# Performance work log

Measured on AMD Instinct MI355X. Metric: run time of the kernel, lower is better.

## Reference

```python
import jax, jax.numpy as jnp
import numpy as np

N, E = 100000, 640000
H, EDGE_D, ATOM_D, RD, L = 128, 10, 25, 64, 4


def _gelu(t):
    return jax.nn.gelu(t, approximate=True)  # tanh approximation, matches torch GELU(approximate='tanh')


def _mlp2(t, w1, b1, w2, b2):
    return _gelu(t @ w1 + b1) @ w2 + b2


def setup_inputs() -> dict:
    key = jax.random.key(0)
    ks = iter(jax.random.split(key, 64))
    s = 0.05
    d = {}
    d['x'] = jax.random.normal(next(ks), (N, ATOM_D), jnp.float32)
    d['edge_index'] = jax.random.randint(next(ks), (2, E), 0, N, jnp.int32)
    d['edge_attr'] = jax.random.normal(next(ks), (E, EDGE_D), jnp.float32)
    d['enc_w1'] = jax.random.normal(next(ks), (ATOM_D, H)) * s
    d['enc_b1'] = jnp.zeros((H,))
    d['enc_w2'] = jax.random.normal(next(ks), (H, H)) * s
    d['enc_b2'] = jnp.zeros((H,))
    d['edge_w1'] = jax.random.normal(next(ks), (L, EDGE_D, H)) * s
    d['edge_b1'] = jnp.zeros((L, H))
    d['edge_w2'] = jax.random.normal(next(ks), (L, H, H)) * s
    d['edge_b2'] = jnp.zeros((L, H))
    d['msg_w1'] = jax.random.normal(next(ks), (L, H, H)) * s
    d['msg_b1'] = jnp.zeros((L, H))
    d['msg_w2'] = jax.random.normal(next(ks), (L, H, H)) * s
    d['msg_b2'] = jnp.zeros((L, H))
    d['gate_w'] = jax.random.normal(next(ks), (L, 2 * H, H)) * s
    d['gate_b'] = jnp.zeros((L, H))
    d['ln_g'] = jnp.ones((L, H))
    d['ln_b'] = jnp.zeros((L, H))
    for name in ('ion', 'pka', 'acid'):
        d[name + '_w1'] = jax.random.normal(next(ks), (H, RD)) * s
        d[name + '_b1'] = jnp.zeros((RD,))
        d[name + '_w2'] = jax.random.normal(next(ks), (RD, 1)) * s
        d[name + '_b2'] = jnp.zeros((1,))
    return d


def reference(x, edge_index, edge_attr, enc_w1, enc_b1, enc_w2, enc_b2,
              edge_w1, edge_b1, edge_w2, edge_b2,
              msg_w1, msg_b1, msg_w2, msg_b2,
              gate_w, gate_b, ln_g, ln_b,
              ion_w1, ion_b1, ion_w2, ion_b2,
              pka_w1, pka_b1, pka_w2, pka_b2,
              acid_w1, acid_b1, acid_w2, acid_b2):
    src, dst = edge_index[0], edge_index[1]
    n = x.shape[0]
    h = _mlp2(x, enc_w1, enc_b1, enc_w2, enc_b2)  # [N, H]
    ones_e = jnp.ones((src.shape[0],), x.dtype)
    count = jnp.clip(jax.ops.segment_sum(ones_e, dst, num_segments=n), 1.0)[:, None]  # [N,1]
    for i in range(L):
        ew = _mlp2(edge_attr, edge_w1[i], edge_b1[i], edge_w2[i], edge_b2[i])  # [E, H]
        msg = _mlp2(h[src], msg_w1[i], msg_b1[i], msg_w2[i], msg_b2[i]) * ew   # [E, H]
        agg = jax.ops.segment_sum(msg, dst, num_segments=n) / count           # [N, H] mean agg
        gate = jax.nn.sigmoid(jnp.concatenate([h, agg], axis=-1) @ gate_w[i] + gate_b[i])
        h = h + gate * agg
        mu = jnp.mean(h, axis=-1, keepdims=True)
        var = jnp.mean(jnp.square(h - mu), axis=-1, keepdims=True)
        h = (h - mu) * jax.lax.rsqrt(var + 1e-5) * ln_g[i] + ln_b[i]
    ion = _mlp2(h, ion_w1, ion_b1, ion_w2, ion_b2)
    pka = _mlp2(h, pka_w1, pka_b1, pka_w2, pka_b2)
    acid = _mlp2(h, acid_w1, acid_b1, acid_w2, acid_b2)
    return (ion, pka, acid)
```

## Files before the change

### kernel.cpp

```cpp
#include <hip/hip_runtime.h>
#include <math.h>

#define NN 100000
#define NN2 100032
#define NE 640000
#define H 128
#define AD 25
#define ED 10
#define RD 64
#define NL 4
#define NB_E (NE / 64 + 1)
#define NSB ((NN + 255) / 256)
#define CAP 256

typedef short bfrag __attribute__((ext_vector_type(8)));
typedef float floatx4 __attribute__((ext_vector_type(4)));
typedef unsigned short ushort;

#define MFMA(a, b, c) __builtin_amdgcn_mfma_f32_16x16x32_bf16(a, b, c, 0, 0, 0)

__device__ __forceinline__ ushort f2bf(float f) {
    unsigned u = __float_as_uint(f);
    unsigned r = (u + 0x7FFFu + ((u >> 16) & 1u)) >> 16;
    return (ushort)r;
}
__device__ __forceinline__ float bf2f(ushort b) {
    return __uint_as_float(((unsigned)b) << 16);
}
__device__ __forceinline__ float gelu_t(float x) {
    float u = 0.7978845608028654f * (x + 0.044715f * x * x * x);
    float e = __expf(2.0f * u);
    float th = 1.0f - 2.0f / (e + 1.0f);
    return 0.5f * x * (1.0f + th);
}
__device__ __forceinline__ float sigm(float x) {
    return 1.0f / (1.0f + __expf(-x));
}

__global__ void k_wtall(ushort* __restrict__ wt,
                        const float* __restrict__ s0, const float* __restrict__ s1,
                        const float* __restrict__ s2, const float* __restrict__ s3,
                        const float* __restrict__ s4, const float* __restrict__ s5,
                        const float* __restrict__ s6, const float* __restrict__ s7,
                        const float* __restrict__ s8, const float* __restrict__ s9) {
    int idx = blockIdx.x * 256 + threadIdx.x;
    const float* src;
    int Ks, N, Kd, off;
    if (idx < 4096)        { src = s0; Ks = 25;  N = 128; Kd = 32;  off = 0; }
    else if (idx < 20480)  { src = s1; Ks = 128; N = 128; Kd = 128; off = 4096; }
    else if (idx < 36864)  { src = s2; Ks = 10;  N = 128; Kd = 32;  off = 20480; }
    else if (idx < 102400) { src = s3; Ks = 128; N = 128; Kd = 128; off = 36864; }
    else if (idx < 167936) { src = s4; Ks = 128; N = 128; Kd = 128; off = 102400; }
    else if (idx < 233472) { src = s5; Ks = 128; N = 128; Kd = 128; off = 167936; }
    else if (idx < 364544) { src = s6; Ks = 256; N = 128; Kd = 256; off = 233472; }
    else if (idx < 372736) { src = s7; Ks = 128; N = 64;  Kd = 128; off = 364544; }
    else if (idx < 380928) { src = s8; Ks = 128; N = 64;  Kd = 128; off = 372736; }
    else if (idx < 389120) { src = s9; Ks = 128; N = 64;  Kd = 128; off = 380928; }
    else return;
    int lidx = idx - off;
    int nk = N * Kd;
    int b = lidx / nk;
    int rem = lidx - b * nk;
    int n = rem / Kd, k = rem - n * Kd;
    float v = (k < Ks) ? src[((size_t)b * Ks + k) * N + n] : 0.0f;
    wt[idx] = f2bf(v);
}

__global__ void k_cvt(const float* __restrict__ src, ushort* __restrict__ dst,
                      int rs, int Ks, int Kd, int total) {
    for (int idx = blockIdx.x * 256 + threadIdx.x; idx < total; idx += gridDim.x * 256) {
        int r = idx / Kd, k = idx - r * Kd;
        dst[idx] = (r < rs && k < Ks) ? f2bf(src[(size_t)r * Ks + k]) : 0;
    }
}
__global__ void k_cvtperm(const float* __restrict__ ea, const int* __restrict__ perm,
                          ushort* __restrict__ out) {
    int j = blockIdx.x * 256 + threadIdx.x;
    if (j >= NE) return;
    const float* src = ea + (size_t)perm[j] * ED;
    unsigned u[8];
#pragma unroll
    for (int k = 0; k < 5; ++k)
        u[k] = (unsigned)f2bf(src[2 * k]) | ((unsigned)f2bf(src[2 * k + 1]) << 16);
    u[5] = u[6] = u[7] = 0u;
    uint4* o = (uint4*)(out + (size_t)j * 16);
    uint4 a; a.x = u[0]; a.y = u[1]; a.z = u[2]; a.w = u[3];
    uint4 b; b.x = u[4]; b.y = u[5]; b.z = u[6]; b.w = u[7];
    o[0] = a; o[1] = b;
}

__global__ void k_init3(int* __restrict__ hist, int* __restrict__ nf,
                        int* __restrict__ nl) {
    int i = blockIdx.x * 256 + threadIdx.x;
    if (i < NN) hist[i] = 0;
    if (i < NB_E) { nf[i] = 0x7fffffff; nl[i] = -1; }
}
__global__ void k_hist(const int* __restrict__ ei, int* __restrict__ hist) {
    int e = blockIdx.x * 256 + threadIdx.x;
    if (e < NE) atomicAdd(&hist[ei[NE + e]], 1);
}
__global__ void k_scan1(const int* __restrict__ hist, int* __restrict__ incl,
                        int* __restrict__ bsum) {
    __shared__ int s[256];
    int tid = threadIdx.x;
    int i = blockIdx.x * 256 + tid;
    s[tid] = (i < NN) ? hist[i] : 0;
    __syncthreads();
    for (int off = 1; off < 256; off <<= 1) {
        int t = (tid >= off) ? s[tid - off] : 0;
        __syncthreads();
        s[tid] += t;
        __syncthreads();
    }
    if (i < NN) incl[i] = s[tid];
    if (tid == 255) bsum[blockIdx.x] = s[255];
}
__global__ void k_scan2(int* __restrict__ bsum) {
    __shared__ int s[512];
    int tid = threadIdx.x;
    s[tid] = (tid < NSB) ? bsum[tid] : 0;
    __syncthreads();
    for (int off = 1; off < 512; off <<= 1) {
        int t = (tid >= off) ? s[tid - off] : 0;
        __syncthreads();
        s[tid] += t;
        __syncthreads();
    }
    if (tid < NSB) bsum[tid] = (tid > 0) ? s[tid - 1] : 0;
}
__global__ void k_scan3(const int* __restrict__ hist, const int* __restrict__ incl,
                        const int* __restrict__ bsum, int* __restrict__ row_ptr) {
    int i = blockIdx.x * 256 + threadIdx.x;
    if (i < NN) row_ptr[i] = bsum[blockIdx.x] + incl[i] - hist[i];
    if (i == 0) row_ptr[NN] = NE;
}
__global__ void k_scatter(const int* __restrict__ ei, int* __restrict__ cursor,
                          int* __restrict__ perm) {
    int e = blockIdx.x * 256 + threadIdx.x;
    if (e < NE) {
        int d = ei[NE + e];
        int pos = atomicAdd(&cursor[d], 1);
        perm[pos] = e;
    }
}
__global__ void k_blockrange(const int* __restrict__ row_ptr, int* __restrict__ nf,
                             int* __restrict__ nl) {
    int n = blockIdx.x * 256 + threadIdx.x;
    if (n < NN) {
        int b = row_ptr[n] >> 6;
        atomicMin(&nf[b], n);
        atomicMax(&nl[b], n);
    }
}

__global__ void __launch_bounds__(256)
k_encmsg(const ushort* __restrict__ xbf, ushort* __restrict__ hbf,
         ushort* __restrict__ mbf,
         const ushort* __restrict__ EW1t, const float* __restrict__ EB1,
         const ushort* __restrict__ EW2t, const float* __restrict__ EB2,
         const ushort* __restrict__ MW1t, const float* __restrict__ MB1,
         const ushort* __restrict__ MW2t, const float* __restrict__ MB2) {
    __shared__ ushort sH[64 * 136];
    const int tid = threadIdx.x;
    const int w = tid >> 6, lane = tid & 63, lr = lane & 15, lg = lane >> 4;
    const int rowB = blockIdx.x * 64 + w * 16 + lr;
    ushort* sHrow = sH + (w * 16 + lr) * 136;

    bfrag bv0 = *(const bfrag*)(xbf + (size_t)rowB * 32 + lg * 8);
    floatx4 acc[8];
#pragma unroll
    for (int t = 0; t < 8; ++t) acc[t] = (floatx4){0.f, 0.f, 0.f, 0.f};
#pragma unroll
    for (int t = 0; t < 8; ++t) {
        bfrag av = *(const bfrag*)(EW1t + (t * 16 + lr) * 32 + lg * 8);
        acc[t] = MFMA(av, bv0, acc[t]);
    }
#pragma unroll
    for (int t = 0; t < 8; ++t) {
        const float4 b1 = *(const float4*)(EB1 + t * 16 + lg * 4);
        float h0 = gelu_t(acc[t][0] + b1.x), h1 = gelu_t(acc[t][1] + b1.y);
        float h2 = gelu_t(acc[t][2] + b1.z), h3 = gelu_t(acc[t][3] + b1.w);
        uint2 p;
        p.x = (unsigned)f2bf(h0) | ((unsigned)f2bf(h1) << 16);
        p.y = (unsigned)f2bf(h2) | ((unsigned)f2bf(h3) << 16);
        *(uint2*)(sHrow + t * 16 + lg * 4) = p;
    }
#pragma unroll
    for (int t = 0; t < 8; ++t) acc[t] = (floatx4){0.f, 0.f, 0.f, 0.f};
#pragma unroll
    for (int kb = 0; kb < 4; ++kb) {
        bfrag av = *(const bfrag*)(sHrow + kb * 32 + lg * 8);
#pragma unroll
        for (int t = 0; t < 8; ++t) {
            bfrag bw = *(const bfrag*)(EW2t + (t * 16 + lr) * 128 + kb * 32 + lg * 8);
            acc[t] = MFMA(bw, av, acc[t]);
        }
    }
#pragma unroll
    for (int t = 0; t < 8; ++t) {
        const float4 b2 = *(const float4*)(EB2 + t * 16 + lg * 4);
        uint2 p;
        p.x = (unsigned)f2bf(acc[t][0] + b2.x) |
              ((unsigned)f2bf(acc[t][1] + b2.y) << 16);
        p.y = (unsigned)f2bf(acc[t][2] + b2.z) |
              ((unsigned)f2bf(acc[t][3] + b2.w) << 16);
        if (rowB < NN) *(uint2*)(hbf + (size_t)rowB * 128 + t * 16 + lg * 4) = p;
        *(uint2*)(sHrow + t * 16 + lg * 4) = p;
    }
#pragma unroll
    for (int t = 0; t < 8; ++t) acc[t] = (floatx4){0.f, 0.f, 0.f, 0.f};
#pragma unroll
    for (int kb = 0; kb < 4; ++kb) {
        bfrag bv = *(const bfrag*)(sHrow + kb * 32 + lg * 8);
#pragma unroll
        for (int t = 0; t < 8; ++t) {
            bfrag av = *(const bfrag*)(MW1t + (t * 16 + lr) * 128 + kb * 32 + lg * 8);
            acc[t] = MFMA(av, bv, acc[t]);
        }
    }
#pragma unroll
    for (int t = 0; t < 8; ++t) {
        const float4 b1 = *(const float4*)(MB1 + t * 16 + lg * 4);
        float h0 = gelu_t(acc[t][0] + b1.x), h1 = gelu_t(acc[t][1] + b1.y);
        float h2 = gelu_t(acc[t][2] + b1.z), h3 = gelu_t(acc[t][3] + b1.w);
        uint2 p;
        p.x = (unsigned)f2bf(h0) | ((unsigned)f2bf(h1) << 16);
        p.y = (unsigned)f2bf(h2) | ((unsigned)f2bf(h3) << 16);
        *(uint2*)(sHrow + t * 16 + lg * 4) = p;
    }
#pragma unroll
    for (int t = 0; t < 8; ++t) acc[t] = (floatx4){0.f, 0.f, 0.f, 0.f};
#pragma unroll
    for (int kb = 0; kb < 4; ++kb) {
        bfrag av = *(const bfrag*)(sHrow + kb * 32 + lg * 8);
#pragma unroll
        for (int t = 0; t < 8; ++t) {
            bfrag bw = *(const bfrag*)(MW2t + (t * 16 + lr) * 128 + kb * 32 + lg * 8);
            acc[t] = MFMA(bw, av, acc[t]);
        }
    }
    if (rowB < NN) {
        ushort* orow = mbf + (size_t)rowB * 128;
#pragma unroll
        for (int t = 0; t < 8; ++t) {
            const float4 b2 = *(const float4*)(MB2 + t * 16 + lg * 4);
            uint2 p;
            p.x = (unsigned)f2bf(acc[t][0] + b2.x) |
                  ((unsigned)f2bf(acc[t][1] + b2.y) << 16);
            p.y = (unsigned)f2bf(acc[t][2] + b2.z) |
                  ((unsigned)f2bf(acc[t][3] + b2.w) << 16);
            *(uint2*)(orow + t * 16 + lg * 4) = p;
        }
    }
}

__global__ void __launch_bounds__(256)
k_ew(const ushort* __restrict__ eap, ushort* __restrict__ ewp, int S,
     const ushort* __restrict__ W1t, const float* __restrict__ B1,
     const ushort* __restrict__ W2t, const float* __restrict__ B2) {
    __shared__ ushort sea[128 * 40];
    __shared__ ushort sH[4][16 * 136];
    const int tid = threadIdx.x;
    const int w = tid >> 6, lane = tid & 63, lr = lane & 15, lg = lane >> 4;
    const int jl0 = blockIdx.x * 128;

    {
        int r = tid >> 1, half = tid & 1;
        int j = S + jl0 + r;
        uint4 z; z.x = z.y = z.z = z.w = 0u;
        uint4 v = z;
        if (j < NE) v = *(const uint4*)(eap + (size_t)j * 16 + half * 8);
        *(uint4*)(sea + r * 40 + half * 8) = v;
        *(uint4*)(sea + r * 40 + 16 + half * 8) = z;
    }
    bfrag av1[8];
#pragma unroll
    for (int t = 0; t < 8; ++t)
        av1[t] = *(const bfrag*)(W1t + (t * 16 + lr) * 32 + lg * 8);
    __syncthreads();

    for (int rt = 0; rt < 2; ++rt) {
        const int row_l = w * 32 + rt * 16;
        floatx4 acc[8];
#pragma unroll
        for (int t = 0; t < 8; ++t) acc[t] = (floatx4){0.f, 0.f, 0.f, 0.f};
        bfrag bv = *(const bfrag*)(sea + (row_l + lr) * 40 + lg * 8);
#pragma unroll
        for (int t = 0; t < 8; ++t) acc[t] = MFMA(av1[t], bv, acc[t]);
        ushort* sHr = sH[w] + lr * 136;
#pragma unroll
        for (int t = 0; t < 8; ++t) {
            const float4 b1 = *(const float4*)(B1 + t * 16 + lg * 4);
            float h0 = gelu_t(acc[t][0] + b1.x), h1 = gelu_t(acc[t][1] + b1.y);
            float h2 = gelu_t(acc[t][2] + b1.z), h3 = gelu_t(acc[t][3] + b1.w);
            uint2 p;
            p.x = (unsigned)f2bf(h0) | ((unsigned)f2bf(h1) << 16);
            p.y = (unsigned)f2bf(h2) | ((unsigned)f2bf(h3) << 16);
            *(uint2*)(sHr + t * 16 + lg * 4) = p;
        }
#pragma unroll
        for (int t = 0; t < 8; ++t) acc[t] = (floatx4){0.f, 0.f, 0.f, 0.f};
#pragma unroll
        for (int kb = 0; kb < 4; ++kb) {
            bfrag av = *(const bfrag*)(sH[w] + lr * 136 + kb * 32 + lg * 8);
#pragma unroll
            for (int t = 0; t < 8; ++t) {
                bfrag bw = *(const bfrag*)(W2t + (t * 16 + lr) * 128 + kb * 32 + lg * 8);
                acc[t] = MFMA(bw, av, acc[t]);
            }
        }
        const int jl = jl0 + row_l + lr;
        if (S + jl < NE) {
            ushort* orow = ewp + (size_t)jl * 128;
#pragma unroll
            for (int t = 0; t < 8; ++t) {
                const float4 b2 = *(const float4*)(B2 + t * 16 + lg * 4);
                uint2 p;
                p.x = (unsigned)f2bf(acc[t][0] + b2.x) |
                      ((unsigned)f2bf(acc[t][1] + b2.y) << 16);
                p.y = (unsigned)f2bf(acc[t][2] + b2.z) |
                      ((unsigned)f2bf(acc[t][3] + b2.w) << 16);
                *(uint2*)(orow + t * 16 + lg * 4) = p;
            }
        }
    }
}

__global__ void __launch_bounds__(256)
k_gms(const int* __restrict__ ei, const int* __restrict__ perm,
      const int* __restrict__ row_ptr, const int* __restrict__ nf,
      const int* __restrict__ nl, const ushort* __restrict__ ewp, int S,
      const ushort* __restrict__ mbf, ushort* __restrict__ aggbf) {
    __shared__ int ssrc[CAP], sdst[CAP], sseg[CAP];
    __shared__ int snode[64];
    __shared__ float sinvd[64];
    __shared__ float sagg[64 * 132];
    __shared__ int swtot[4];
    __shared__ int s_nseg;

    const int b = blockIdx.x;
    const int n0 = nf[b];
    if (n0 >= NN) return;
    const int n1 = nl[b];
    const int e0 = row_ptr[n0];
    int ne = row_ptr[n1 + 1] - e0;
    if (ne <= 0) return;
    const int ncl = (ne < CAP) ? ne : CAP;

    const int tid = threadIdx.x;
    const int w = tid >> 6, lane = tid & 63;

    for (int i = tid; i < 64 * 132; i += 256) sagg[i] = 0.0f;

    int dstv = -1 - tid;
    if (tid < ncl) {
        int e = perm[e0 + tid];
        ssrc[tid] = ei[e];
        dstv = ei[NE + e];
    }
    sdst[tid] = dstv;
    __syncthreads();

    int f = 0;
    if (tid < ncl) f = (tid == 0) ? 1 : (sdst[tid] != sdst[tid - 1]);
    unsigned long long mk = __ballot(f);
    int incl = __popcll(mk & (~0ull >> (63 - lane)));
    if (lane == 63) swtot[w] = incl;
    __syncthreads();
    int woff = 0;
    for (int i = 0; i < w; ++i) woff += swtot[i];
    int segid = woff + incl;
    sseg[tid] = segid - 1;
    if (f) {
        int s = segid - 1;
        snode[s] = dstv;
        sinvd[s] = 1.0f / (float)(row_ptr[dstv + 1] - row_ptr[dstv]);
    }
    if (tid == 255) s_nseg = segid;
    __syncthreads();
    const int nseg = s_nseg;

    const int c0 = (tid & 31) * 4;
    const int g = tid >> 5;
    const int chunk = (ncl + 7) >> 3;
    const int j0 = g * chunk;
    const int j1 = (j0 + chunk < ncl) ? (j0 + chunk) : ncl;
    const int be = e0 - S;
    int cs = -1;
    float v0 = 0.f, v1 = 0.f, v2 = 0.f, v3 = 0.f;
    uint2 ewc, mvc;
    if (j0 < j1) {
        ewc = *(const uint2*)(ewp + (size_t)(be + j0) * 128 + c0);
        mvc = *(const uint2*)(mbf + (size_t)ssrc[j0] * 128 + c0);
    }
    for (int j = j0; j < j1; ++j) {
        uint2 ewn = ewc, mvn = mvc;
        if (j + 1 < j1) {
            ewn = *(const uint2*)(ewp + (size_t)(be + j + 1) * 128 + c0);
            mvn = *(const uint2*)(mbf + (size_t)ssrc[j + 1] * 128 + c0);
        }
        float a0 = bf2f((ushort)(ewc.x & 0xFFFF)) * bf2f((ushort)(mvc.x & 0xFFFF));
        float a1 = bf2f((ushort)(ewc.x >> 16)) * bf2f((ushort)(mvc.x >> 16));
        float a2 = bf2f((ushort)(ewc.y & 0xFFFF)) * bf2f((ushort)(mvc.y & 0xFFFF));
        float a3 = bf2f((ushort)(ewc.y >> 16)) * bf2f((ushort)(mvc.y >> 16));
        int sg = sseg[j];
        if (sg != cs) {
            if (cs >= 0) {
                float* p = &sagg[cs * 132 + c0];
                atomicAdd(p + 0, v0); atomicAdd(p + 1, v1);
                atomicAdd(p + 2, v2); atomicAdd(p + 3, v3);
            }
            cs = sg; v0 = a0; v1 = a1; v2 = a2; v3 = a3;
        } else {
            v0 += a0; v1 += a1; v2 += a2; v3 += a3;
        }
        ewc = ewn; mvc = mvn;
    }
    if (cs >= 0) {
        float* p = &sagg[cs * 132 + c0];
        atomicAdd(p + 0, v0); atomicAdd(p + 1, v1);
        atomicAdd(p + 2, v2); atomicAdd(p + 3, v3);
    }
    __syncthreads();
    for (int i = tid; i < nseg * 32; i += 256) {
        int s = i >> 5, qd = i & 31;
        float inv = sinvd[s];
        const float* p = &sagg[s * 132 + qd * 4];
        uint2 pk;
        pk.x = (unsigned)f2bf(p[0] * inv) | ((unsigned)f2bf(p[1] * inv) << 16);
        pk.y = (unsigned)f2bf(p[2] * inv) | ((unsigned)f2bf(p[3] * inv) << 16);
        *(uint2*)(aggbf + (size_t)snode[s] * 128 + qd * 4) = pk;
    }
}

__global__ void __launch_bounds__(256)
k_gatemlp(ushort* __restrict__ hbf, const ushort* __restrict__ aggbf,
          const ushort* __restrict__ GWt, const float* __restrict__ GB,
          const float* __restrict__ LNG, const float* __restrict__ LNB,
          const ushort* __restrict__ W1t, const float* __restrict__ B1,
          const ushort* __restrict__ W2t, const float* __restrict__ B2,
          ushort* __restrict__ mbf) {
    __shared__ ushort sA[64 * 136];
    const int tid = threadIdx.x;
    const int w = tid >> 6, lane = tid & 63, lr = lane & 15, lg = lane >> 4;
    const int row = blockIdx.x * 64 + w * 16 + lr;

    bfrag bvv[8];
    uint2 hp[8], ap[8];
#pragma unroll
    for (int kb = 0; kb < 4; ++kb)
        bvv[kb] = *(const bfrag*)(hbf + (size_t)row * 128 + kb * 32 + lg * 8);
#pragma unroll
    for (int kb = 0; kb < 4; ++kb)
        bvv[4 + kb] = *(const bfrag*)(aggbf + (size_t)row * 128 + kb * 32 + lg * 8);
#pragma unroll
    for (int t = 0; t < 8; ++t) {
        hp[t] = *(const uint2*)(hbf + (size_t)row * 128 + t * 16 + lg * 4);
        ap[t] = *(const uint2*)(aggbf + (size_t)row * 128 + t * 16 + lg * 4);
    }

    floatx4 acc[8];
#pragma unroll
    for (int t = 0; t < 8; ++t) acc[t] = (floatx4){0.f, 0.f, 0.f, 0.f};
#pragma unroll
    for (int kb = 0; kb < 8; ++kb) {
#pragma unroll
        for (int t = 0; t < 8; ++t) {
            bfrag av = *(const bfrag*)(GWt + (t * 16 + lr) * 256 + kb * 32 + lg * 8);
            acc[t] = MFMA(av, bvv[kb], acc[t]);
        }
    }
    float o[8][4];
    float s = 0.0f;
#pragma unroll
    for (int t = 0; t < 8; ++t) {
        const int c0 = t * 16 + lg * 4;
        const float4 gb = *(const float4*)(GB + c0);
        float h0 = bf2f((ushort)(hp[t].x & 0xFFFF)), h1 = bf2f((ushort)(hp[t].x >> 16));
        float h2 = bf2f((ushort)(hp[t].y & 0xFFFF)), h3 = bf2f((ushort)(hp[t].y >> 16));
        float a0 = bf2f((ushort)(ap[t].x & 0xFFFF)), a1 = bf2f((ushort)(ap[t].x >> 16));
        float a2 = bf2f((ushort)(ap[t].y & 0xFFFF)), a3 = bf2f((ushort)(ap[t].y >> 16));
        o[t][0] = h0 + sigm(acc[t][0] + gb.x) * a0;
        o[t][1] = h1 + sigm(acc[t][1] + gb.y) * a1;
        o[t][2] = h2 + sigm(acc[t][2] + gb.z) * a2;
        o[t][3] = h3 + sigm(acc[t][3] + gb.w) * a3;
        s += o[t][0] + o[t][1] + o[t][2] + o[t][3];
    }
    s += __shfl_xor(s, 16);
    s += __shfl_xor(s, 32);
    const float mu = s * (1.0f / 128.0f);
    float q = 0.0f;
#pragma unroll
    for (int t = 0; t < 8; ++t)
#pragma unroll
        for (int r = 0; r < 4; ++r) {
            float dx = o[t][r] - mu;
            q = fmaf(dx, dx, q);
        }
    q += __shfl_xor(q, 16);
    q += __shfl_xor(q, 32);
    const float rs = rsqrtf(q * (1.0f / 128.0f) + 1e-5f);

    ushort* sArow = sA + (w * 16 + lr) * 136;
#pragma unroll
    for (int t = 0; t < 8; ++t) {
        const int c0 = t * 16 + lg * 4;
        const float4 g4 = *(const float4*)(LNG + c0);
        const float4 b4 = *(const float4*)(LNB + c0);
        float r0 = fmaf((o[t][0] - mu) * rs, g4.x, b4.x);
        float r1 = fmaf((o[t][1] - mu) * rs, g4.y, b4.y);
        float r2 = fmaf((o[t][2] - mu) * rs, g4.z, b4.z);
        float r3 = fmaf((o[t][3] - mu) * rs, g4.w, b4.w);
        uint2 pk;
        pk.x = (unsigned)f2bf(r0) | ((unsigned)f2bf(r1) << 16);
        pk.y = (unsigned)f2bf(r2) | ((unsigned)f2bf(r3) << 16);
        if (row < NN) *(uint2*)(hbf + (size_t)row * 128 + c0) = pk;
        *(uint2*)(sArow + c0) = pk;
    }

#pragma unroll
    for (int t = 0; t < 8; ++t) acc[t] = (floatx4){0.f, 0.f, 0.f, 0.f};
#pragma unroll
    for (int kb = 0; kb < 4; ++kb) {
        bfrag bv = *(const bfrag*)(sArow + kb * 32 + lg * 8);
#pragma unroll
        for (int t = 0; t < 8; ++t) {
            bfrag av = *(const bfrag*)(W1t + (t * 16 + lr) * 128 + kb * 32 + lg * 8);
            acc[t] = MFMA(av, bv, acc[t]);
        }
    }
#pragma unroll
    for (int t = 0; t < 8; ++t) {
        const float4 b1 = *(const float4*)(B1 + t * 16 + lg * 4);
        float h0 = gelu_t(acc[t][0] + b1.x), h1 = gelu_t(acc[t][1] + b1.y);
        float h2 = gelu_t(acc[t][2] + b1.z), h3 = gelu_t(acc[t][3] + b1.w);
        uint2 p;
        p.x = (unsigned)f2bf(h0) | ((unsigned)f2bf(h1) << 16);
        p.y = (unsigned)f2bf(h2) | ((unsigned)f2bf(h3) << 16);
        *(uint2*)(sArow + t * 16 + lg * 4) = p;
    }
#pragma unroll
    for (int t = 0; t < 8; ++t) acc[t] = (floatx4){0.f, 0.f, 0.f, 0.f};
#pragma unroll
    for (int kb = 0; kb < 4; ++kb) {
        bfrag av = *(const bfrag*)(sArow + kb * 32 + lg * 8);
#pragma unroll
        for (int t = 0; t < 8; ++t) {
            bfrag bw = *(const bfrag*)(W2t + (t * 16 + lr) * 128 + kb * 32 + lg * 8);
            acc[t] = MFMA(bw, av, acc[t]);
        }
    }
    if (row < NN) {
        ushort* orow = mbf + (size_t)row * 128;
#pragma unroll
        for (int t = 0; t < 8; ++t) {
            const float4 b2 = *(const float4*)(B2 + t * 16 + lg * 4);
            uint2 p;
            p.x = (unsigned)f2bf(acc[t][0] + b2.x) |
                  ((unsigned)f2bf(acc[t][1] + b2.y) << 16);
            p.y = (unsigned)f2bf(acc[t][2] + b2.z) |
                  ((unsigned)f2bf(acc[t][3] + b2.w) << 16);
            *(uint2*)(orow + t * 16 + lg * 4) = p;
        }
    }
}

__global__ void __launch_bounds__(256)
k_gateheads(const ushort* __restrict__ hbf, const ushort* __restrict__ aggbf,
            const ushort* __restrict__ GWt, const float* __restrict__ GB,
            const float* __restrict__ LNG, const float* __restrict__ LNB,
            const ushort* __restrict__ WHt, float* __restrict__ OUT,
            const float* __restrict__ b1a, const float* __restrict__ b1b,
            const float* __restrict__ b1c,
            const float* __restrict__ w2a, const float* __restrict__ w2b,
            const float* __restrict__ w2c,
            const float* __restrict__ b2a, const float* __restrict__ b2b,
            const float* __restrict__ b2c) {
    __shared__ ushort sA[64 * 136];
    const int tid = threadIdx.x;
    const int w = tid >> 6, lane = tid & 63, lr = lane & 15, lg = lane >> 4;
    const int row = blockIdx.x * 64 + w * 16 + lr;

    bfrag bvv[8];
    uint2 hp[8], ap[8];
#pragma unroll
    for (int kb = 0; kb < 4; ++kb)
        bvv[kb] = *(const bfrag*)(hbf + (size_t)row * 128 + kb * 32 + lg * 8);
#pragma unroll
    for (int kb = 0; kb < 4; ++kb)
        bvv[4 + kb] = *(const bfrag*)(aggbf + (size_t)row * 128 + kb * 32 + lg * 8);
#pragma unroll
    for (int t = 0; t < 8; ++t) {
        hp[t] = *(const uint2*)(hbf + (size_t)row * 128 + t * 16 + lg * 4);
        ap[t] = *(const uint2*)(aggbf + (size_t)row * 128 + t * 16 + lg * 4);
    }

    floatx4 acc[8];
#pragma unroll
    for (int t = 0; t < 8; ++t) acc[t] = (floatx4){0.f, 0.f, 0.f, 0.f};
#pragma unroll
    for (int kb = 0; kb < 8; ++kb) {
#pragma unroll
        for (int t = 0; t < 8; ++t) {
            bfrag av = *(const bfrag*)(GWt + (t * 16 + lr) * 256 + kb * 32 + lg * 8);
            acc[t] = MFMA(av, bvv[kb], acc[t]);
        }
    }
    float o[8][4];
    float s = 0.0f;
#pragma unroll
    for (int t = 0; t < 8; ++t) {
        const int c0 = t * 16 + lg * 4;
        const float4 gb = *(const float4*)(GB + c0);
        float h0 = bf2f((ushort)(hp[t].x & 0xFFFF)), h1 = bf2f((ushort)(hp[t].x >> 16));
        float h2 = bf2f((ushort)(hp[t].y & 0xFFFF)), h3 = bf2f((ushort)(hp[t].y >> 16));
        float a0 = bf2f((ushort)(ap[t].x & 0xFFFF)), a1 = bf2f((ushort)(ap[t].x >> 16));
        float a2 = bf2f((ushort)(ap[t].y & 0xFFFF)), a3 = bf2f((ushort)(ap[t].y >> 16));
        o[t][0] = h0 + sigm(acc[t][0] + gb.x) * a0;
        o[t][1] = h1 + sigm(acc[t][1] + gb.y) * a1;
        o[t][2] = h2 + sigm(acc[t][2] + gb.z) * a2;
        o[t][3] = h3 + sigm(acc[t][3] + gb.w) * a3;
        s += o[t][0] + o[t][1] + o[t][2] + o[t][3];
    }
    s += __shfl_xor(s, 16);
    s += __shfl_xor(s, 32);
    const float mu = s * (1.0f / 128.0f);
    float q = 0.0f;
#pragma unroll
    for (int t = 0; t < 8; ++t)
#pragma unroll
        for (int r = 0; r < 4; ++r) {
            float dx = o[t][r] - mu;
            q = fmaf(dx, dx, q);
        }
    q += __shfl_xor(q, 16);
    q += __shfl_xor(q, 32);
    const float rs = rsqrtf(q * (1.0f / 128.0f) + 1e-5f);

    ushort* sArow = sA + (w * 16 + lr) * 136;
#pragma unroll
    for (int t = 0; t < 8; ++t) {
        const int c0 = t * 16 + lg * 4;
        const float4 g4 = *(const float4*)(LNG + c0);
        const float4 b4 = *(const float4*)(LNB + c0);
        float r0 = fmaf((o[t][0] - mu) * rs, g4.x, b4.x);
        float r1 = fmaf((o[t][1] - mu) * rs, g4.y, b4.y);
        float r2 = fmaf((o[t][2] - mu) * rs, g4.z, b4.z);
        float r3 = fmaf((o[t][3] - mu) * rs, g4.w, b4.w);
        uint2 pk;
        pk.x = (unsigned)f2bf(r0) | ((unsigned)f2bf(r1) << 16);
        pk.y = (unsigned)f2bf(r2) | ((unsigned)f2bf(r3) << 16);
        *(uint2*)(sArow + c0) = pk;
    }

    floatx4 acc2[12];
#pragma unroll
    for (int t = 0; t < 12; ++t) acc2[t] = (floatx4){0.f, 0.f, 0.f, 0.f};
#pragma unroll
    for (int kb = 0; kb < 4; ++kb) {
        bfrag bv = *(const bfrag*)(sArow + kb * 32 + lg * 8);
#pragma unroll
        for (int t = 0; t < 12; ++t) {
            bfrag av = *(const bfrag*)(WHt + (t * 16 + lr) * 128 + kb * 32 + lg * 8);
            acc2[t] = MFMA(av, bv, acc2[t]);
        }
    }
    const float* b1s[3] = {b1a, b1b, b1c};
    const float* w2s[3] = {w2a, w2b, w2c};
    float p[3] = {0.f, 0.f, 0.f};
#pragma unroll
    for (int t = 0; t < 12; ++t) {
        const int head = t >> 2;
        const int c0 = (t & 3) * 16 + lg * 4;
        const float4 b1 = *(const float4*)(b1s[head] + c0);
        const float4 w2 = *(const float4*)(w2s[head] + c0);
        p[head] += gelu_t(acc2[t][0] + b1.x) * w2.x;
        p[head] += gelu_t(acc2[t][1] + b1.y) * w2.y;
        p[head] += gelu_t(acc2[t][2] + b1.z) * w2.z;
        p[head] += gelu_t(acc2[t][3] + b1.w) * w2.w;
    }
#pragma unroll
    for (int hd = 0; hd < 3; ++hd) {
        p[hd] += __shfl_xor(p[hd], 16);
        p[hd] += __shfl_xor(p[hd], 32);
    }
    if (lg == 0 && row < NN) {
        OUT[0 * NN + row] = p[0] + b2a[0];
        OUT[1 * NN + row] = p[1] + b2b[0];
        OUT[2 * NN + row] = p[2] + b2c[0];
    }
}

extern "C" void kernel_launch(void* const* d_in, const int* in_sizes, int n_in,
                              void* d_out, int out_size, void* d_ws, size_t ws_size,
                              hipStream_t stream) {
    const float* x       = (const float*)d_in[0];
    const int*   ei      = (const int*)d_in[1];
    const float* ea      = (const float*)d_in[2];
    const float* enc_w1  = (const float*)d_in[3];
    const float* enc_b1  = (const float*)d_in[4];
    const float* enc_w2  = (const float*)d_in[5];
    const float* enc_b2  = (const float*)d_in[6];
    const float* edge_w1 = (const float*)d_in[7];
    const float* edge_b1 = (const float*)d_in[8];
    const float* edge_w2 = (const float*)d_in[9];
    const float* edge_b2 = (const float*)d_in[10];
    const float* msg_w1  = (const float*)d_in[11];
    const float* msg_b1  = (const float*)d_in[12];
    const float* msg_w2  = (const float*)d_in[13];
    const float* msg_b2  = (const float*)d_in[14];
    const float* gate_w  = (const float*)d_in[15];
    const float* gate_b  = (const float*)d_in[16];
    const float* ln_g    = (const float*)d_in[17];
    const float* ln_b    = (const float*)d_in[18];
    const float* hw[12];
    for (int t = 0; t < 12; ++t) hw[t] = (const float*)d_in[19 + t];

    const size_t NNH = (size_t)NN2 * H;
    ushort* hbf   = (ushort*)d_ws;
    ushort* mbf   = hbf + NNH;
    ushort* aggbf = mbf + NNH;
    ushort* xbf   = aggbf + NNH;
    ushort* eapbf = xbf + (size_t)NN2 * 32;
    ushort* wt    = eapbf + (size_t)NE * 16;
    ushort* wt_enc1 = wt;
    ushort* wt_enc2 = wt_enc1 + 128 * 32;
    ushort* wt_e1   = wt_enc2 + 128 * 128;
    ushort* wt_e2   = wt_e1 + 4 * 128 * 32;
    ushort* wt_m1   = wt_e2 + 4 * 128 * 128;
    ushort* wt_m2   = wt_m1 + 4 * 128 * 128;
    ushort* wt_g    = wt_m2 + 4 * 128 * 128;
    ushort* wt_h    = wt_g + 4 * 128 * 256;
    int* row_ptr = (int*)(wt_h + 192 * 128 + 64);
    int* perm    = row_ptr + 100352;
    int* nf      = perm + NE;
    int* nl      = nf + 10240;
    int* hist    = nl + 10240;
    int* incl    = hist + 100352;
    int* cursor  = incl + 100352;
    int* bsum    = cursor + 100352;
    uintptr_t ewp_addr = ((uintptr_t)(bsum + 512) + 15) & ~(uintptr_t)15;
    ushort* ewp = (ushort*)ewp_addr;
    const size_t used = ewp_addr - (uintptr_t)d_ws;

    int P = 4;
    size_t rows = NE / 4 + 1024;
    if (ws_size >= used + (size_t)NE * 128 * 2) { P = 1; rows = NE; }
    else if (ws_size >= used + ((size_t)NE / 2 + 1024) * 128 * 2) { P = 2; rows = NE / 2 + 1024; }
    const int PE = NE / P;
    const int NGB = 10000 / P;
    const int ewblk = (int)(rows / 128);

    k_init3<<<(NN + 255) / 256, 256, 0, stream>>>(hist, nf, nl);
    hipMemsetAsync(aggbf, 0, NNH * sizeof(ushort), stream);
    k_hist<<<(NE + 255) / 256, 256, 0, stream>>>(ei, hist);
    k_scan1<<<NSB, 256, 0, stream>>>(hist, incl, bsum);
    k_scan2<<<1, 512, 0, stream>>>(bsum);
    k_scan3<<<NSB, 256, 0, stream>>>(hist, incl, bsum, row_ptr);
    hipMemcpyAsync(cursor, row_ptr, NN * sizeof(int), hipMemcpyDeviceToDevice, stream);
    k_scatter<<<(NE + 255) / 256, 256, 0, stream>>>(ei, cursor, perm);
    k_blockrange<<<(NN + 255) / 256, 256, 0, stream>>>(row_ptr, nf, nl);

    k_wtall<<<1520, 256, 0, stream>>>(wt, enc_w1, enc_w2, edge_w1, edge_w2,
                                      msg_w1, msg_w2, gate_w, hw[0], hw[4], hw[8]);
    k_cvt<<<3200, 256, 0, stream>>>(x, xbf, NN, 25, 32, NN2 * 32);
    k_cvtperm<<<(NE + 255) / 256, 256, 0, stream>>>(ea, perm, eapbf);

    const int ntiles = NN2 / 64;
    k_encmsg<<<ntiles, 256, 0, stream>>>(xbf, hbf, mbf,
        wt_enc1, enc_b1, wt_enc2, enc_b2,
        wt_m1, msg_b1, wt_m2, msg_b2);

    for (int l = 0; l < NL; ++l) {
        for (int p = 0; p < P; ++p) {
            const int S = p * PE;
            k_ew<<<ewblk, 256, 0, stream>>>(eapbf, ewp, S,
                wt_e1 + (size_t)l * 128 * 32, edge_b1 + l * H,
                wt_e2 + (size_t)l * 128 * 128, edge_b2 + l * H);
            const int nb = (p == P - 1) ? (NGB + 1) : NGB;
            k_gms<<<nb, 256, 0, stream>>>(ei, perm, row_ptr,
                nf + p * NGB, nl + p * NGB, ewp, S, mbf, aggbf);
        }
        if (l < NL - 1) {
            k_gatemlp<<<ntiles, 256, 0, stream>>>(hbf, aggbf,
                wt_g + (size_t)l * 128 * 256, gate_b + l * H,
                ln_g + l * H, ln_b + l * H,
                wt_m1 + (size_t)(l + 1) * 128 * 128, msg_b1 + (l + 1) * H,
                wt_m2 + (size_t)(l + 1) * 128 * 128, msg_b2 + (l + 1) * H, mbf);
        } else {
            k_gateheads<<<ntiles, 256, 0, stream>>>(hbf, aggbf,
                wt_g + (size_t)l * 128 * 256, gate_b + l * H,
                ln_g + l * H, ln_b + l * H,
                wt_h, (float*)d_out,
                hw[1], hw[5], hw[9], hw[2], hw[6], hw[10], hw[3], hw[7], hw[11]);
        }
    }
}
```

Baseline: 2.195 ms.

## Fuse graph preprocessing into one cooperative kernel with grid syncs

Measured after the change: 2.813 ms. 1.28x slower.

```diff
diff --git a/kernel.cpp b/kernel.cpp
--- a/kernel.cpp
+++ b/kernel.cpp
@@ -1,5 +1,8 @@
 #include <hip/hip_runtime.h>
+#include <hip/hip_cooperative_groups.h>
 #include <math.h>
+
+namespace cg = cooperative_groups;
 
 #define NN 100000
 #define NN2 100032
@@ -37,13 +40,108 @@
     return 1.0f / (1.0f + __expf(-x));
 }
 
-__global__ void k_wtall(ushort* __restrict__ wt,
+__global__ void k_prep(const int* __restrict__ ei, const float* __restrict__ ea,
+                       int* __restrict__ hist, int* __restrict__ incl,
+                       int* __restrict__ bsum, int* __restrict__ row_ptr,
+                       int* __restrict__ cursor, int* __restrict__ perm,
+                       int* __restrict__ nf, int* __restrict__ nl,
+                       ushort* __restrict__ eapbf, ushort* __restrict__ aggbf) {
+    cg::grid_group grid = cg::this_grid();
+    __shared__ int s[512];
+    const int tid = threadIdx.x;
+    const int gtid = blockIdx.x * 256 + tid;
+    const int gsz = gridDim.x * 256;
+
+    for (int i = gtid; i < NN; i += gsz) hist[i] = 0;
+    for (int i = gtid; i < NB_E; i += gsz) { nf[i] = 0x7fffffff; nl[i] = -1; }
+    uint4 z; z.x = z.y = z.z = z.w = 0u;
+    for (int i = gtid; i < NN2 * 16; i += gsz) ((uint4*)aggbf)[i] = z;
+    grid.sync();
+
+    for (int e = gtid; e < NE; e += gsz) atomicAdd(&hist[ei[NE + e]], 1);
+    grid.sync();
+
+    if (blockIdx.x < NSB) {
+        int i = blockIdx.x * 256 + tid;
+        s[tid] = (i < NN) ? hist[i] : 0;
+        __syncthreads();
+        for (int off = 1; off < 256; off <<= 1) {
+            int t = (tid >= off) ? s[tid - off] : 0;
+            __syncthreads();
+            s[tid] += t;
+            __syncthreads();
+        }
+        if (i < NN) incl[i] = s[tid];
+        if (tid == 255) bsum[blockIdx.x] = s[255];
+    }
+    grid.sync();
+
+    if (blockIdx.x == 0) {
+        s[tid] = (tid < NSB) ? bsum[tid] : 0;
+        s[tid + 256] = (tid + 256 < NSB) ? bsum[tid + 256] : 0;
+        __syncthreads();
+        for (int off = 1; off < 512; off <<= 1) {
+            int v0 = (tid >= off) ? s[tid - off] : 0;
+            int v1 = (tid + 256 >= off) ? s[tid + 256 - off] : 0;
+            __syncthreads();
+            s[tid] += v0;
+            s[tid + 256] += v1;
+            __syncthreads();
+        }
+        if (tid < NSB) bsum[tid] = (tid > 0) ? s[tid - 1] : 0;
+        if (tid + 256 < NSB) bsum[tid + 256] = s[tid + 255];
+    }
+    grid.sync();
+
+    for (int i = gtid; i < NN; i += gsz) {
+        int rp = bsum[i >> 8] + incl[i] - hist[i];
+        row_ptr[i] = rp;
+        cursor[i] = rp;
+    }
+    if (gtid == 0) row_ptr[NN] = NE;
+    grid.sync();
+
+    for (int e = gtid; e < NE; e += gsz) {
+        int d = ei[NE + e];
+        int pos = atomicAdd(&cursor[d], 1);
+        perm[pos] = e;
+    }
+    grid.sync();
+
+    for (int n = gtid; n < NN; n += gsz) {
+        int b = row_ptr[n] >> 6;
+        atomicMin(&nf[b], n);
+        atomicMax(&nl[b], n);
+    }
+    for (int j = gtid; j < NE; j += gsz) {
+        const float* src = ea + (size_t)perm[j] * ED;
+        unsigned u[8];
+#pragma unroll
+        for (int k = 0; k < 5; ++k)
+            u[k] = (unsigned)f2bf(src[2 * k]) | ((unsigned)f2bf(src[2 * k + 1]) << 16);
+        u[5] = u[6] = u[7] = 0u;
+        uint4* o = (uint4*)(eapbf + (size_t)j * 16);
+        uint4 a; a.x = u[0]; a.y = u[1]; a.z = u[2]; a.w = u[3];
+        uint4 b; b.x = u[4]; b.y = u[5]; b.z = u[6]; b.w = u[7];
+        o[0] = a; o[1] = b;
+    }
+}
+
+__global__ void k_wtall(ushort* __restrict__ wt, ushort* __restrict__ xbf,
+                        const float* __restrict__ x,
                         const float* __restrict__ s0, const float* __restrict__ s1,
                         const float* __restrict__ s2, const float* __restrict__ s3,
                         const float* __restrict__ s4, const float* __restrict__ s5,
                         const float* __restrict__ s6, const float* __restrict__ s7,
                         const float* __restrict__ s8, const float* __restrict__ s9) {
     int idx = blockIdx.x * 256 + threadIdx.x;
+    if (idx >= 389120) {
+        int lidx = idx - 389120;
+        if (lidx >= NN2 * 32) return;
+        int r = lidx >> 5, k = lidx & 31;
+        xbf[lidx] = (r < NN && k < 25) ? f2bf(x[(size_t)r * 25 + k]) : 0;
+        return;
+    }
     const float* src;
     int Ks, N, Kd, off;
     if (idx < 4096)        { src = s0; Ks = 25;  N = 128; Kd = 32;  off = 0; }
@@ -55,8 +153,7 @@
     else if (idx < 364544) { src = s6; Ks = 256; N = 128; Kd = 256; off = 233472; }
     else if (idx < 372736) { src = s7; Ks = 128; N = 64;  Kd = 128; off = 364544; }
     else if (idx < 380928) { src = s8; Ks = 128; N = 64;  Kd = 128; off = 372736; }
-    else if (idx < 389120) { src = s9; Ks = 128; N = 64;  Kd = 128; off = 380928; }
-    else return;
+    else                   { src = s9; Ks = 128; N = 64;  Kd = 128; off = 380928; }
     int lidx = idx - off;
     int nk = N * Kd;
     int b = lidx / nk;
@@ -64,93 +161,6 @@
     int n = rem / Kd, k = rem - n * Kd;
     float v = (k < Ks) ? src[((size_t)b * Ks + k) * N + n] : 0.0f;
     wt[idx] = f2bf(v);
-}
-
-__global__ void k_cvt(const float* __restrict__ src, ushort* __restrict__ dst,
-                      int rs, int Ks, int Kd, int total) {
-    for (int idx = blockIdx.x * 256 + threadIdx.x; idx < total; idx += gridDim.x * 256) {
-        int r = idx / Kd, k = idx - r * Kd;
-        dst[idx] = (r < rs && k < Ks) ? f2bf(src[(size_t)r * Ks + k]) : 0;
-    }
-}
-__global__ void k_cvtperm(const float* __restrict__ ea, const int* __restrict__ perm,
-                          ushort* __restrict__ out) {
-    int j = blockIdx.x * 256 + threadIdx.x;
-    if (j >= NE) return;
-    const float* src = ea + (size_t)perm[j] * ED;
-    unsigned u[8];
-#pragma unroll
-    for (int k = 0; k < 5; ++k)
-        u[k] = (unsigned)f2bf(src[2 * k]) | ((unsigned)f2bf(src[2 * k + 1]) << 16);
-    u[5] = u[6] = u[7] = 0u;
-    uint4* o = (uint4*)(out + (size_t)j * 16);
-    uint4 a; a.x = u[0]; a.y = u[1]; a.z = u[2]; a.w = u[3];
-    uint4 b; b.x = u[4]; b.y = u[5]; b.z = u[6]; b.w = u[7];
-    o[0] = a; o[1] = b;
-}
-
-__global__ void k_init3(int* __restrict__ hist, int* __restrict__ nf,
-                        int* __restrict__ nl) {
-    int i = blockIdx.x * 256 + threadIdx.x;
-    if (i < NN) hist[i] = 0;
-    if (i < NB_E) { nf[i] = 0x7fffffff; nl[i] = -1; }
-}
-__global__ void k_hist(const int* __restrict__ ei, int* __restrict__ hist) {
-    int e = blockIdx.x * 256 + threadIdx.x;
-    if (e < NE) atomicAdd(&hist[ei[NE + e]], 1);
-}
-__global__ void k_scan1(const int* __restrict__ hist, int* __restrict__ incl,
-                        int* __restrict__ bsum) {
-    __shared__ int s[256];
-    int tid = threadIdx.x;
-    int i = blockIdx.x * 256 + tid;
-    s[tid] = (i < NN) ? hist[i] : 0;
-    __syncthreads();
-    for (int off = 1; off < 256; off <<= 1) {
-        int t = (tid >= off) ? s[tid - off] : 0;
-        __syncthreads();
-        s[tid] += t;
-        __syncthreads();
-    }
-    if (i < NN) incl[i] = s[tid];
-    if (tid == 255) bsum[blockIdx.x] = s[255];
-}
-__global__ void k_scan2(int* __restrict__ bsum) {
-    __shared__ int s[512];
-    int tid = threadIdx.x;
-    s[tid] = (tid < NSB) ? bsum[tid] : 0;
-    __syncthreads();
-    for (int off = 1; off < 512; off <<= 1) {
-        int t = (tid >= off) ? s[tid - off] : 0;
-        __syncthreads();
-        s[tid] += t;
-        __syncthreads();
-    }
-    if (tid < NSB) bsum[tid] = (tid > 0) ? s[tid - 1] : 0;
-}
-__global__ void k_scan3(const int* __restrict__ hist, const int* __restrict__ incl,
-                        const int* __restrict__ bsum, int* __restrict__ row_ptr) {
-    int i = blockIdx.x * 256 + threadIdx.x;
-    if (i < NN) row_ptr[i] = bsum[blockIdx.x] + incl[i] - hist[i];
-    if (i == 0) row_ptr[NN] = NE;
-}
-__global__ void k_scatter(const int* __restrict__ ei, int* __restrict__ cursor,
-                          int* __restrict__ perm) {
-    int e = blockIdx.x * 256 + threadIdx.x;
-    if (e < NE) {
-        int d = ei[NE + e];
-        int pos = atomicAdd(&cursor[d], 1);
-        perm[pos] = e;
-    }
-}
-__global__ void k_blockrange(const int* __restrict__ row_ptr, int* __restrict__ nf,
-                             int* __restrict__ nl) {
-    int n = blockIdx.x * 256 + threadIdx.x;
-    if (n < NN) {
-        int b = row_ptr[n] >> 6;
-        atomicMin(&nf[b], n);
-        atomicMax(&nl[b], n);
-    }
 }
 
 __global__ void __launch_bounds__(256)
@@ -751,20 +761,18 @@
     const int NGB = 10000 / P;
     const int ewblk = (int)(rows / 128);
 
-    k_init3<<<(NN + 255) / 256, 256, 0, stream>>>(hist, nf, nl);
-    hipMemsetAsync(aggbf, 0, NNH * sizeof(ushort), stream);
-    k_hist<<<(NE + 255) / 256, 256, 0, stream>>>(ei, hist);
-    k_scan1<<<NSB, 256, 0, stream>>>(hist, incl, bsum);
-    k_scan2<<<1, 512, 0, stream>>>(bsum);
-    k_scan3<<<NSB, 256, 0, stream>>>(hist, incl, bsum, row_ptr);
-    hipMemcpyAsync(cursor, row_ptr, NN * sizeof(int), hipMemcpyDeviceToDevice, stream);
-    k_scatter<<<(NE + 255) / 256, 256, 0, stream>>>(ei, cursor, perm);
-    k_blockrange<<<(NN + 255) / 256, 256, 0, stream>>>(row_ptr, nf, nl);
-
-    k_wtall<<<1520, 256, 0, stream>>>(wt, enc_w1, enc_w2, edge_w1, edge_w2,
-                                      msg_w1, msg_w2, gate_w, hw[0], hw[4], hw[8]);
-    k_cvt<<<3200, 256, 0, stream>>>(x, xbf, NN, 25, 32, NN2 * 32);
-    k_cvtperm<<<(NE + 255) / 256, 256, 0, stream>>>(ea, perm, eapbf);
+    {
+        void* args[] = {
+            (void*)&ei, (void*)&ea, (void*)&hist, (void*)&incl, (void*)&bsum,
+            (void*)&row_ptr, (void*)&cursor, (void*)&perm, (void*)&nf, (void*)&nl,
+            (void*)&eapbf, (void*)&aggbf
+        };
+        hipLaunchCooperativeKernel((const void*)k_prep, dim3(1024), dim3(256),
+                                   args, 0, stream);
+    }
+
+    k_wtall<<<14024, 256, 0, stream>>>(wt, xbf, x, enc_w1, enc_w2, edge_w1, edge_w2,
+                                       msg_w1, msg_w2, gate_w, hw[0], hw[4], hw[8]);
 
     const int ntiles = NN2 / 64;
     k_encmsg<<<ntiles, 256, 0, stream>>>(xbf, hbf, mbf,
```
